# Optimization experiments

Measured on AMD Instinct MI355X. Metric: run time of the kernel, lower is better.

Reference implementation:

```python
import jax, jax.numpy as jnp
import numpy as np

NUM_NODES = 50000
NUM_EDGES = 800000
NUM_GRAPHS = 1024
D_IN = 64
D_PROT = 1280
HID = 256
OUT = 1


def setup_inputs() -> dict:
    key = jax.random.key(0)
    ks = jax.random.split(key, 16)
    s = 0.02
    x = jax.random.normal(ks[0], (NUM_NODES, D_IN), dtype=jnp.float32)
    edge_index = jax.random.randint(ks[1], (2, NUM_EDGES), 0, NUM_NODES, dtype=jnp.int32)
    batch = jnp.sort(jax.random.randint(ks[2], (NUM_NODES,), 0, NUM_GRAPHS, dtype=jnp.int32))
    protein_embedding = jax.random.normal(ks[3], (NUM_GRAPHS, D_PROT), dtype=jnp.float32)
    # SAGEConv params: lin_l (aggregated neighbors, with bias), lin_r (self, no bias)
    Wl = jax.random.normal(ks[4], (D_IN, HID), dtype=jnp.float32) * s
    bl = jnp.zeros((HID,), dtype=jnp.float32)
    Wr = jax.random.normal(ks[5], (D_IN, HID), dtype=jnp.float32) * s
    Wp = jax.random.normal(ks[6], (D_PROT, HID), dtype=jnp.float32) * s
    bp = jnp.zeros((HID,), dtype=jnp.float32)
    Wi = jax.random.normal(ks[7], (2 * HID, HID), dtype=jnp.float32) * s
    bi = jnp.zeros((HID,), dtype=jnp.float32)
    Wo = jax.random.normal(ks[8], (HID, OUT), dtype=jnp.float32) * s
    bo = jnp.zeros((OUT,), dtype=jnp.float32)
    return {"x": x, "protein_embedding": protein_embedding, "Wl": Wl, "bl": bl,
            "Wr": Wr, "Wp": Wp, "bp": bp, "Wi": Wi, "bi": bi, "Wo": Wo, "bo": bo,
            "edge_index": edge_index, "batch": batch}


def _segment_mean(vals, seg_ids, num_segments):
    sums = jax.ops.segment_sum(vals, seg_ids, num_segments=num_segments)
    cnt = jax.ops.segment_sum(jnp.ones((vals.shape[0],), vals.dtype), seg_ids,
                              num_segments=num_segments)
    return sums / jnp.maximum(cnt, 1.0)[:, None]


def reference(x, protein_embedding, Wl, bl, Wr, Wp, bp, Wi, bi, Wo, bo, edge_index, batch):
    src, dst = edge_index[0], edge_index[1]
    # SAGEConv: mean-aggregate neighbor messages at target nodes, then fuse linears
    aggr = _segment_mean(x[src], dst, NUM_NODES)           # [N, D_IN]
    drug_x = jax.nn.relu(aggr @ Wl + bl + x @ Wr)          # [N, HID]
    # global_mean_pool over graphs in the batch
    pooled = _segment_mean(drug_x, batch, NUM_GRAPHS)      # [G, HID]
    protein_x = protein_embedding @ Wp + bp                # [G, HID]
    combined = jnp.concatenate((pooled, protein_x), axis=1)  # [G, 2*HID]
    interaction = jax.nn.relu(combined @ Wi + bi)          # [G, HID]
    return interaction @ Wo + bo                           # [G, OUT]
```

## Files before the change

### kernel.cpp

```cpp
#include <hip/hip_runtime.h>
#include <hip/hip_bf16.h>

#define N_NODES 50000
#define N_EDGES 800000
#define N_GRAPHS 1024
#define D_IN 64
#define D_PROT 1280
#define HID 256
#define N_PAD 50048

#define NB 782
#define BCAP 2048
#define BEPB 4096
#define BBLK 196

typedef __attribute__((ext_vector_type(8))) short short8;
typedef __attribute__((ext_vector_type(4))) float f32x4;
typedef __hip_bfloat16 bf16;

__device__ inline unsigned bf16rne(float f) {
  unsigned u = __float_as_uint(f);
  return (u + 0x7fffu + ((u >> 16) & 1u)) >> 16;
}
__device__ inline void acc_bf2(float4& a, uint2 v) {
  a.x += __uint_as_float(v.x << 16);
  a.y += __uint_as_float(v.x & 0xffff0000u);
  a.z += __uint_as_float(v.y << 16);
  a.w += __uint_as_float(v.y & 0xffff0000u);
}

#define PREP_XC 3125
#define PREP_PE (PREP_XC + 1280)
#define PREP_PL (PREP_PE + 8)
#define PREP_PR (PREP_PL + 8)
#define PREP_WP (PREP_PR + 160)
#define PREP_WI (PREP_WP + 64)

__device__ inline void pack_frag(const float* __restrict__ src, bf16* __restrict__ dst,
                                 int KC, int tid) {
  int lane = tid & 63;
  int chunk = tid >> 6;
  int c = chunk / KC, kc = chunk - c * KC;
  int kbase = kc * 32 + ((lane >> 4) * 8);
  int n = c * 16 + (lane & 15);
#pragma unroll
  for (int j = 0; j < 8; ++j)
    dst[(size_t)tid * 8 + j] = __float2bfloat16(src[(size_t)(kbase + j) * HID + n]);
}

__global__ __launch_bounds__(256) void k_front(
    const float* __restrict__ x, const float* __restrict__ pe,
    const float* __restrict__ Wl, const float* __restrict__ Wr,
    const float* __restrict__ Wp, const float* __restrict__ Wi,
    const int* __restrict__ ei,
    uint2* __restrict__ x2, uint2* __restrict__ pe2,
    bf16* __restrict__ Wl_pk, bf16* __restrict__ Wr_pk,
    bf16* __restrict__ Wp_pk, bf16* __restrict__ Wi_pk,
    int* __restrict__ bcnt, unsigned* __restrict__ bped) {
  __shared__ int hist[NB];
  __shared__ int base[NB];
  const int b = blockIdx.x;
  const int t = threadIdx.x;
  if (b < BBLK) {
    const int e0 = b * BEPB;
    for (int i = t; i < NB; i += 256) hist[i] = 0;
    __syncthreads();
    for (int i = t; i < BEPB; i += 1024) {
      int d[4]; bool v[4];
#pragma unroll
      for (int u = 0; u < 4; ++u) {
        int idx = i + u * 256;
        v[u] = (e0 + idx < N_EDGES);
        d[u] = v[u] ? ei[N_EDGES + e0 + idx] : 0;
      }
#pragma unroll
      for (int u = 0; u < 4; ++u)
        if (v[u]) atomicAdd(&hist[d[u] >> 6], 1);
    }
    __syncthreads();
    for (int i = t; i < NB; i += 256) {
      int c = hist[i];
      base[i] = (c > 0) ? atomicAdd(&bcnt[i], c) : 0;
      hist[i] = 0;
    }
    __syncthreads();
    for (int i = t; i < BEPB; i += 1024) {
      int s[4], d[4]; bool v[4];
#pragma unroll
      for (int u = 0; u < 4; ++u) {
        int idx = i + u * 256;
        v[u] = (e0 + idx < N_EDGES);
        s[u] = v[u] ? ei[e0 + idx] : 0;
        d[u] = v[u] ? ei[N_EDGES + e0 + idx] : 0;
      }
#pragma unroll
      for (int u = 0; u < 4; ++u) {
        if (v[u]) {
          int bk = d[u] >> 6;
          int pos = base[bk] + atomicAdd(&hist[bk], 1);
          if (pos < BCAP)
            bped[(size_t)bk * BCAP + pos] =
                (unsigned)s[u] | ((unsigned)(d[u] & 63) << 16);
        }
      }
    }
    return;
  }
  const int pb = b - BBLK;
  if (pb < PREP_XC) {
    int tid = pb * 256 + t;
    float4 v = ((const float4*)x)[tid];
    x2[tid] = make_uint2(bf16rne(v.x) | (bf16rne(v.y) << 16),
                         bf16rne(v.z) | (bf16rne(v.w) << 16));
  } else if (pb < PREP_PE) {
    int tid = (pb - PREP_XC) * 256 + t;
    float4 v = ((const float4*)pe)[tid];
    pe2[tid] = make_uint2(bf16rne(v.x) | (bf16rne(v.y) << 16),
                          bf16rne(v.z) | (bf16rne(v.w) << 16));
  } else if (pb < PREP_PL) {
    pack_frag(Wl, Wl_pk, 2, (pb - PREP_PE) * 256 + t);
  } else if (pb < PREP_PR) {
    pack_frag(Wr, Wr_pk, 2, (pb - PREP_PL) * 256 + t);
  } else if (pb < PREP_WP) {
    pack_frag(Wp, Wp_pk, 40, (pb - PREP_PR) * 256 + t);
  } else {
    pack_frag(Wi, Wi_pk, 16, (pb - PREP_WP) * 256 + t);
  }
}

__global__ __launch_bounds__(256) void k_mid(
    const uint2* __restrict__ x2, const unsigned* __restrict__ bped,
    const int* __restrict__ bcnt, uint2* __restrict__ a2,
    const bf16* __restrict__ pebf, const bf16* __restrict__ Wp_pk,
    float* __restrict__ prot4) {
  __shared__ unsigned s_raw[BCAP];
  __shared__ unsigned short s_e[BCAP];
  __shared__ int s_off[65];
  __shared__ int s_cur[64];
  const int t = threadIdx.x;
  if (blockIdx.x < NB) {
    const int b = blockIdx.x;
    const int nE = min(bcnt[b], BCAP);
    if (t < 64) s_cur[t] = 0;
    __syncthreads();
    for (int i = t; i < nE; i += 256) {
      unsigned pk = bped[(size_t)b * BCAP + i];
      s_raw[i] = pk;
      atomicAdd(&s_cur[(pk >> 16) & 63], 1);
    }
    __syncthreads();
    if (t < 64) {
      int sc = s_cur[t];
#pragma unroll
      for (int off = 1; off < 64; off <<= 1) {
        int u = __shfl_up(sc, off);
        if (t >= off) sc += u;
      }
      s_off[t + 1] = sc;
      if (t == 0) s_off[0] = 0;
      s_cur[t] = 0;
    }
    __syncthreads();
    for (int i = t; i < nE; i += 256) {
      unsigned pk = s_raw[i];
      int ld = (pk >> 16) & 63;
      int pos = s_off[ld] + atomicAdd(&s_cur[ld], 1);
      s_e[pos] = (unsigned short)(pk & 0xffffu);
    }
    __syncthreads();

    const int w = t >> 6, lane = t & 63;
    const int el = lane >> 4;
    const int fb = lane & 15;
    for (int n = w; n < 64; n += 4) {
      const int beg = s_off[n], end = s_off[n + 1];
      float4 s0 = {0,0,0,0}, s1 = {0,0,0,0}, s2 = {0,0,0,0}, s3 = {0,0,0,0};
      int e = beg;
      for (; e + 16 <= end; e += 16) {
        int i0 = s_e[e + el],     i1 = s_e[e + 4 + el];
        int i2 = s_e[e + 8 + el], i3 = s_e[e + 12 + el];
        uint2 v0 = x2[(size_t)i0 * 16 + fb];
        uint2 v1 = x2[(size_t)i1 * 16 + fb];
        uint2 v2 = x2[(size_t)i2 * 16 + fb];
        uint2 v3 = x2[(size_t)i3 * 16 + fb];
        acc_bf2(s0, v0); acc_bf2(s1, v1); acc_bf2(s2, v2); acc_bf2(s3, v3);
      }
      for (; e + 4 <= end; e += 4)
        acc_bf2(s0, x2[(size_t)s_e[e + el] * 16 + fb]);
      if (e + el < end)
        acc_bf2(s1, x2[(size_t)s_e[e + el] * 16 + fb]);
      float4 tt;
      tt.x = (s0.x + s1.x) + (s2.x + s3.x);
      tt.y = (s0.y + s1.y) + (s2.y + s3.y);
      tt.z = (s0.z + s1.z) + (s2.z + s3.z);
      tt.w = (s0.w + s1.w) + (s2.w + s3.w);
      tt.x += __shfl_xor(tt.x, 32); tt.x += __shfl_xor(tt.x, 16);
      tt.y += __shfl_xor(tt.y, 32); tt.y += __shfl_xor(tt.y, 16);
      tt.z += __shfl_xor(tt.z, 32); tt.z += __shfl_xor(tt.z, 16);
      tt.w += __shfl_xor(tt.w, 32); tt.w += __shfl_xor(tt.w, 16);
      const int node = b * 64 + n;
      if (el == 0 && node < N_NODES) {
        float inv = 1.0f / (float)max(end - beg, 1);
        uint2 o;
        o.x = bf16rne(tt.x * inv) | (bf16rne(tt.y * inv) << 16);
        o.y = bf16rne(tt.z * inv) | (bf16rne(tt.w * inv) << 16);
        a2[(size_t)node * 16 + fb] = o;
      }
    }
    return;
  }
  const int kb = blockIdx.x - NB;
  const int w = t >> 6, lane = t & 63;
  const int ml = lane & 15, q = lane >> 4;
  const int mt = kb >> 2, ks = kb & 3;
  const int g0 = mt * 16, kc0 = ks * 10;
  f32x4 acc[4];
#pragma unroll
  for (int c = 0; c < 4; ++c) acc[c] = (f32x4){0.f, 0.f, 0.f, 0.f};
  for (int kc = kc0; kc < kc0 + 10; ++kc) {
    short8 a = *(const short8*)(pebf + (size_t)(g0 + ml) * D_PROT + kc * 32 + q * 8);
#pragma unroll
    for (int cl = 0; cl < 4; ++cl) {
      short8 bb = *(const short8*)(Wp_pk + ((size_t)((w * 4 + cl) * 40 + kc) * 64 + lane) * 8);
      acc[cl] = __builtin_amdgcn_mfma_f32_16x16x32_bf16(a, bb, acc[cl], 0, 0, 0);
    }
  }
#pragma unroll
  for (int cl = 0; cl < 4; ++cl) {
    const int col = w * 64 + cl * 16 + ml;
#pragma unroll
    for (int i = 0; i < 4; ++i)
      prot4[((size_t)ks * N_GRAPHS + g0 + q * 4 + i) * HID + col] = acc[cl][i];
  }
}

__global__ __launch_bounds__(256) void k_mlp(
    const bf16* __restrict__ aggrbf, const bf16* __restrict__ xbf,
    const bf16* __restrict__ Wl_pk, const bf16* __restrict__ Wr_pk,
    const float* __restrict__ bl, unsigned short* __restrict__ drug) {
  const int t = threadIdx.x, w = t >> 6, lane = t & 63;
  const int ml = lane & 15, q = lane >> 4;
  const int n0 = blockIdx.x * 64;

  f32x4 acc[4][4];
#pragma unroll
  for (int a = 0; a < 4; ++a)
#pragma unroll
    for (int c = 0; c < 4; ++c) acc[a][c] = (f32x4){0.f, 0.f, 0.f, 0.f};

#pragma unroll
  for (int mat = 0; mat < 2; ++mat) {
    const bf16* A = mat ? xbf : aggrbf;
    const bf16* B = mat ? Wr_pk : Wl_pk;
#pragma unroll
    for (int kc = 0; kc < 2; ++kc) {
      short8 af[4], bfr[4];
#pragma unroll
      for (int rt = 0; rt < 4; ++rt)
        af[rt] = *(const short8*)(A + (size_t)(n0 + rt * 16 + ml) * D_IN + kc * 32 + q * 8);
#pragma unroll
      for (int cl = 0; cl < 4; ++cl)
        bfr[cl] = *(const short8*)(B + ((size_t)((w * 4 + cl) * 2 + kc) * 64 + lane) * 8);
#pragma unroll
      for (int rt = 0; rt < 4; ++rt)
#pragma unroll
        for (int cl = 0; cl < 4; ++cl)
          acc[rt][cl] = __builtin_amdgcn_mfma_f32_16x16x32_bf16(af[rt], bfr[cl], acc[rt][cl], 0, 0, 0);
    }
  }

#pragma unroll
  for (int cl = 0; cl < 4; ++cl) {
    const int col = w * 64 + cl * 16 + ml;
    const float bias = bl[col];
#pragma unroll
    for (int rt = 0; rt < 4; ++rt) {
#pragma unroll
      for (int i = 0; i < 4; ++i) {
        const int row = n0 + rt * 16 + q * 4 + i;
        drug[(size_t)row * HID + col] =
            (unsigned short)bf16rne(fmaxf(acc[rt][cl][i] + bias, 0.f));
      }
    }
  }
}

__device__ inline int lb_dev(const int* __restrict__ a, int v) {
  int lo = 0, hi = N_NODES;
  while (lo < hi) { int m = (lo + hi) >> 1; if (a[m] < v) lo = m + 1; else hi = m; }
  return lo;
}

__global__ __launch_bounds__(256) void k_pool(
    const unsigned short* __restrict__ drug, const int* __restrict__ batch,
    const float* __restrict__ prot4, const float* __restrict__ bp,
    unsigned short* __restrict__ comb) {
  const int t = threadIdx.x;
  if (blockIdx.x < N_GRAPHS) {
    const int g = blockIdx.x;
    const int lo = lb_dev(batch, g);
    const int hi = lb_dev(batch, g + 1);
    float s0 = 0.f, s1 = 0.f, s2 = 0.f, s3 = 0.f;
    float s4 = 0.f, s5 = 0.f, s6 = 0.f, s7 = 0.f;
    int r = lo;
    for (; r + 8 <= hi; r += 8) {
      s0 += __uint_as_float((unsigned)drug[(size_t)(r + 0) * HID + t] << 16);
      s1 += __uint_as_float((unsigned)drug[(size_t)(r + 1) * HID + t] << 16);
      s2 += __uint_as_float((unsigned)drug[(size_t)(r + 2) * HID + t] << 16);
      s3 += __uint_as_float((unsigned)drug[(size_t)(r + 3) * HID + t] << 16);
      s4 += __uint_as_float((unsigned)drug[(size_t)(r + 4) * HID + t] << 16);
      s5 += __uint_as_float((unsigned)drug[(size_t)(r + 5) * HID + t] << 16);
      s6 += __uint_as_float((unsigned)drug[(size_t)(r + 6) * HID + t] << 16);
      s7 += __uint_as_float((unsigned)drug[(size_t)(r + 7) * HID + t] << 16);
    }
    for (; r < hi; ++r)
      s0 += __uint_as_float((unsigned)drug[(size_t)r * HID + t] << 16);
    float inv = 1.0f / (float)max(hi - lo, 1);
    float m = (((s0 + s1) + (s2 + s3)) + ((s4 + s5) + (s6 + s7))) * inv;
    comb[(size_t)g * 512 + t] = (unsigned short)bf16rne(m);
    return;
  }
  const int pb = blockIdx.x - N_GRAPHS;
#pragma unroll
  for (int g = 0; g < 4; ++g) {
    const int gg = pb * 4 + g;
    size_t idx = (size_t)gg * HID + t;
    float pr = prot4[idx] + prot4[(size_t)N_GRAPHS * HID + idx]
             + prot4[2 * (size_t)N_GRAPHS * HID + idx]
             + prot4[3 * (size_t)N_GRAPHS * HID + idx];
    comb[(size_t)gg * 512 + HID + t] = (unsigned short)bf16rne(pr + bp[t]);
  }
}

__global__ __launch_bounds__(256) void k_tail(
    const bf16* __restrict__ comb, const bf16* __restrict__ Wi_pk,
    const float* __restrict__ bi, const float* __restrict__ Wo,
    const float* __restrict__ bo, float* __restrict__ out) {
  __shared__ float sRed[16 * 4];
  const int t = threadIdx.x, w = t >> 6, lane = t & 63;
  const int ml = lane & 15, q = lane >> 4;
  const int g0 = blockIdx.x * 16;
  f32x4 acc[4];
#pragma unroll
  for (int c = 0; c < 4; ++c) acc[c] = (f32x4){0.f, 0.f, 0.f, 0.f};
  for (int kc = 0; kc < 16; ++kc) {
    short8 a = *(const short8*)(comb + (size_t)(g0 + ml) * 512 + kc * 32 + q * 8);
#pragma unroll
    for (int cl = 0; cl < 4; ++cl) {
      short8 bb = *(const short8*)(Wi_pk + ((size_t)((w * 4 + cl) * 16 + kc) * 64 + lane) * 8);
      acc[cl] = __builtin_amdgcn_mfma_f32_16x16x32_bf16(a, bb, acc[cl], 0, 0, 0);
    }
  }
  float bic[4], woc[4];
#pragma unroll
  for (int cl = 0; cl < 4; ++cl) {
    const int col = w * 64 + cl * 16 + ml;
    bic[cl] = bi[col];
    woc[cl] = Wo[col];
  }
#pragma unroll
  for (int i = 0; i < 4; ++i) {
    float s = 0.f;
#pragma unroll
    for (int cl = 0; cl < 4; ++cl)
      s += fmaxf(acc[cl][i] + bic[cl], 0.f) * woc[cl];
    s += __shfl_xor(s, 1); s += __shfl_xor(s, 2);
    s += __shfl_xor(s, 4); s += __shfl_xor(s, 8);
    if (ml == 0) sRed[(q * 4 + i) * 4 + w] = s;
  }
  __syncthreads();
  if (t < 16)
    out[g0 + t] = sRed[t * 4 + 0] + sRed[t * 4 + 1] + sRed[t * 4 + 2]
                + sRed[t * 4 + 3] + bo[0];
}

extern "C" void kernel_launch(void* const* d_in, const int* in_sizes, int n_in,
                              void* d_out, int out_size, void* d_ws, size_t ws_size,
                              hipStream_t stream) {
  const float* x     = (const float*)d_in[0];
  const float* pe    = (const float*)d_in[1];
  const float* Wl    = (const float*)d_in[2];
  const float* bl    = (const float*)d_in[3];
  const float* Wr    = (const float*)d_in[4];
  const float* Wp    = (const float*)d_in[5];
  const float* bp    = (const float*)d_in[6];
  const float* Wi    = (const float*)d_in[7];
  const float* bi    = (const float*)d_in[8];
  const float* Wo    = (const float*)d_in[9];
  const float* bo    = (const float*)d_in[10];
  const int*   ei    = (const int*)d_in[11];
  const int*   batch = (const int*)d_in[12];
  float* out = (float*)d_out;

  char* p = (char*)d_ws;
  auto alloc = [&](size_t bytes) {
    char* r = p;
    p += (bytes + 255) & ~(size_t)255;
    return r;
  };
  int*      bcnt  = (int*)alloc(NB * 4);
  size_t zbytes = (size_t)(p - (char*)d_ws);
  unsigned* bped  = (unsigned*)alloc((size_t)NB * BCAP * 4);
  bf16*  xbf    = (bf16*)alloc((size_t)N_PAD * D_IN * 2);
  bf16*  aggrbf = (bf16*)alloc((size_t)N_PAD * D_IN * 2);
  bf16*  pebf   = (bf16*)alloc((size_t)N_GRAPHS * D_PROT * 2);
  bf16*  Wl_pk  = (bf16*)alloc((size_t)D_IN * HID * 2);
  bf16*  Wr_pk  = (bf16*)alloc((size_t)D_IN * HID * 2);
  bf16*  Wp_pk  = (bf16*)alloc((size_t)D_PROT * HID * 2);
  bf16*  Wi_pk  = (bf16*)alloc((size_t)2 * HID * HID * 2);
  float* prot4  = (float*)alloc((size_t)4 * N_GRAPHS * HID * 4);
  unsigned short* drug = (unsigned short*)alloc((size_t)N_PAD * HID * 2);
  unsigned short* comb = (unsigned short*)alloc((size_t)N_GRAPHS * 2 * HID * 2);

  (void)hipMemsetAsync(d_ws, 0, zbytes, stream);

  k_front<<<BBLK + PREP_WI, 256, 0, stream>>>(
      x, pe, Wl, Wr, Wp, Wi, ei,
      (uint2*)xbf, (uint2*)pebf, Wl_pk, Wr_pk, Wp_pk, Wi_pk, bcnt, bped);
  k_mid<<<NB + 256, 256, 0, stream>>>(
      (const uint2*)xbf, bped, bcnt, (uint2*)aggrbf, pebf, Wp_pk, prot4);
  k_mlp<<<N_PAD / 64, 256, 0, stream>>>(aggrbf, xbf, Wl_pk, Wr_pk, bl, drug);
  k_pool<<<N_GRAPHS + 256, 256, 0, stream>>>(drug, batch, prot4, bp, comb);
  k_tail<<<N_GRAPHS / 16, 256, 0, stream>>>((const bf16*)comb, Wi_pk, bi, Wo, bo, out);
}
```

Before: 173.2 us.

## Fuse SAGE linear and mean pooling into aggregation kernel via atomics

The aggregation kernel now keeps the per-node mean aggregate in shared memory and immediately runs the Wl/Wr MFMA GEMM, applying bias and ReLU. It then reduces rows per graph and atomically adds them into a float pool-sum buffer. The protein-sum and mean normalization are folded into the tail kernel, which builds the combined row tile in LDS. This removes the aggr, drug and comb intermediate buffers and two kernel launches, in exchange for more LDS and register pressure in k_mid and contention from atomic adds into poolsum.

New measurement: 167.4 us. 3.3% less time.

```diff
diff --git a/kernel.cpp b/kernel.cpp
--- a/kernel.cpp
+++ b/kernel.cpp
@@ -128,18 +128,23 @@
   }
 }
 
-__global__ __launch_bounds__(256) void k_mid(
+__global__ __launch_bounds__(256, 4) void k_mid(
     const uint2* __restrict__ x2, const unsigned* __restrict__ bped,
-    const int* __restrict__ bcnt, uint2* __restrict__ a2,
+    const int* __restrict__ bcnt, const int* __restrict__ batch,
+    const bf16* __restrict__ Wl_pk, const bf16* __restrict__ Wr_pk,
+    const float* __restrict__ bl, float* __restrict__ poolsum,
     const bf16* __restrict__ pebf, const bf16* __restrict__ Wp_pk,
     float* __restrict__ prot4) {
-  __shared__ unsigned s_raw[BCAP];
+  __shared__ unsigned s_raw[2304];
   __shared__ unsigned short s_e[BCAP];
   __shared__ int s_off[65];
   __shared__ int s_cur[64];
+  __shared__ int s_batch[64];
   const int t = threadIdx.x;
   if (blockIdx.x < NB) {
+    uint2* aggT = (uint2*)s_raw;
     const int b = blockIdx.x;
+    const int n0 = b * 64;
     const int nE = min(bcnt[b], BCAP);
     if (t < 64) s_cur[t] = 0;
     __syncthreads();
@@ -166,6 +171,10 @@
       int ld = (pk >> 16) & 63;
       int pos = s_off[ld] + atomicAdd(&s_cur[ld], 1);
       s_e[pos] = (unsigned short)(pk & 0xffffu);
+    }
+    if (t < 64) {
+      int node = n0 + t;
+      s_batch[t] = (node < N_NODES) ? batch[node] : 0x7fffffff;
     }
     __syncthreads();
 
@@ -198,13 +207,63 @@
       tt.y += __shfl_xor(tt.y, 32); tt.y += __shfl_xor(tt.y, 16);
       tt.z += __shfl_xor(tt.z, 32); tt.z += __shfl_xor(tt.z, 16);
       tt.w += __shfl_xor(tt.w, 32); tt.w += __shfl_xor(tt.w, 16);
-      const int node = b * 64 + n;
-      if (el == 0 && node < N_NODES) {
+      if (el == 0) {
         float inv = 1.0f / (float)max(end - beg, 1);
         uint2 o;
         o.x = bf16rne(tt.x * inv) | (bf16rne(tt.y * inv) << 16);
         o.y = bf16rne(tt.z * inv) | (bf16rne(tt.w * inv) << 16);
-        a2[(size_t)node * 16 + fb] = o;
+        aggT[n * 18 + fb] = o;
+      }
+    }
+    __syncthreads();
+
+    const int ml = lane & 15, q = lane >> 4;
+    const int lv = min(63, N_NODES - 1 - n0);
+    float bic[4];
+#pragma unroll
+    for (int cl = 0; cl < 4; ++cl) bic[cl] = bl[w * 64 + cl * 16 + ml];
+#pragma unroll
+    for (int rt = 0; rt < 4; ++rt) {
+      f32x4 acc[4];
+#pragma unroll
+      for (int cl = 0; cl < 4; ++cl) acc[cl] = (f32x4){0.f, 0.f, 0.f, 0.f};
+      const int arow = rt * 16 + ml;
+#pragma unroll
+      for (int kc = 0; kc < 2; ++kc) {
+        short8 a0 = *(const short8*)(&aggT[arow * 18 + kc * 8 + q * 2]);
+#pragma unroll
+        for (int cl = 0; cl < 4; ++cl) {
+          short8 bb = *(const short8*)(Wl_pk + ((size_t)((w * 4 + cl) * 2 + kc) * 64 + lane) * 8);
+          acc[cl] = __builtin_amdgcn_mfma_f32_16x16x32_bf16(a0, bb, acc[cl], 0, 0, 0);
+        }
+        short8 a1 = *(const short8*)((const bf16*)x2 + (size_t)(n0 + arow) * D_IN + kc * 32 + q * 8);
+#pragma unroll
+        for (int cl = 0; cl < 4; ++cl) {
+          short8 bb = *(const short8*)(Wr_pk + ((size_t)((w * 4 + cl) * 2 + kc) * 64 + lane) * 8);
+          acc[cl] = __builtin_amdgcn_mfma_f32_16x16x32_bf16(a1, bb, acc[cl], 0, 0, 0);
+        }
+      }
+      float vv[4][4];
+      int bt[4];
+#pragma unroll
+      for (int i = 0; i < 4; ++i) bt[i] = s_batch[rt * 16 + q * 4 + i];
+#pragma unroll
+      for (int cl = 0; cl < 4; ++cl)
+#pragma unroll
+        for (int i = 0; i < 4; ++i)
+          vv[cl][i] = fmaxf(acc[cl][i] + bic[cl], 0.f);
+      const int glo = s_batch[min(rt * 16, lv)];
+      const int ghi = s_batch[min(rt * 16 + 15, lv)];
+      for (int g = glo; g <= ghi; ++g) {
+#pragma unroll
+        for (int cl = 0; cl < 4; ++cl) {
+          float s = 0.f;
+#pragma unroll
+          for (int i = 0; i < 4; ++i) s += (bt[i] == g) ? vv[cl][i] : 0.f;
+          s += __shfl_xor(s, 16); s += __shfl_xor(s, 32);
+          if (q == 0)
+            atomicAdd(&poolsum[(size_t)g * HID + (w * 64 + cl * 16 + ml)], s);
+        }
       }
     }
     return;
@@ -234,117 +293,49 @@
   }
 }
 
-__global__ __launch_bounds__(256) void k_mlp(
-    const bf16* __restrict__ aggrbf, const bf16* __restrict__ xbf,
-    const bf16* __restrict__ Wl_pk, const bf16* __restrict__ Wr_pk,
-    const float* __restrict__ bl, unsigned short* __restrict__ drug) {
-  const int t = threadIdx.x, w = t >> 6, lane = t & 63;
-  const int ml = lane & 15, q = lane >> 4;
-  const int n0 = blockIdx.x * 64;
-
-  f32x4 acc[4][4];
-#pragma unroll
-  for (int a = 0; a < 4; ++a)
-#pragma unroll
-    for (int c = 0; c < 4; ++c) acc[a][c] = (f32x4){0.f, 0.f, 0.f, 0.f};
-
-#pragma unroll
-  for (int mat = 0; mat < 2; ++mat) {
-    const bf16* A = mat ? xbf : aggrbf;
-    const bf16* B = mat ? Wr_pk : Wl_pk;
-#pragma unroll
-    for (int kc = 0; kc < 2; ++kc) {
-      short8 af[4], bfr[4];
-#pragma unroll
-      for (int rt = 0; rt < 4; ++rt)
-        af[rt] = *(const short8*)(A + (size_t)(n0 + rt * 16 + ml) * D_IN + kc * 32 + q * 8);
-#pragma unroll
-      for (int cl = 0; cl < 4; ++cl)
-        bfr[cl] = *(const short8*)(B + ((size_t)((w * 4 + cl) * 2 + kc) * 64 + lane) * 8);
-#pragma unroll
-      for (int rt = 0; rt < 4; ++rt)
-#pragma unroll
-        for (int cl = 0; cl < 4; ++cl)
-          acc[rt][cl] = __builtin_amdgcn_mfma_f32_16x16x32_bf16(af[rt], bfr[cl], acc[rt][cl], 0, 0, 0);
-    }
-  }
-
-#pragma unroll
-  for (int cl = 0; cl < 4; ++cl) {
-    const int col = w * 64 + cl * 16 + ml;
-    const float bias = bl[col];
-#pragma unroll
-    for (int rt = 0; rt < 4; ++rt) {
-#pragma unroll
-      for (int i = 0; i < 4; ++i) {
-        const int row = n0 + rt * 16 + q * 4 + i;
-        drug[(size_t)row * HID + col] =
-            (unsigned short)bf16rne(fmaxf(acc[rt][cl][i] + bias, 0.f));
-      }
-    }
-  }
-}
-
 __device__ inline int lb_dev(const int* __restrict__ a, int v) {
   int lo = 0, hi = N_NODES;
   while (lo < hi) { int m = (lo + hi) >> 1; if (a[m] < v) lo = m + 1; else hi = m; }
   return lo;
 }
 
-__global__ __launch_bounds__(256) void k_pool(
-    const unsigned short* __restrict__ drug, const int* __restrict__ batch,
+__global__ __launch_bounds__(256) void k_tail(
+    const float* __restrict__ poolsum, const int* __restrict__ batch,
     const float* __restrict__ prot4, const float* __restrict__ bp,
-    unsigned short* __restrict__ comb) {
-  const int t = threadIdx.x;
-  if (blockIdx.x < N_GRAPHS) {
-    const int g = blockIdx.x;
-    const int lo = lb_dev(batch, g);
-    const int hi = lb_dev(batch, g + 1);
-    float s0 = 0.f, s1 = 0.f, s2 = 0.f, s3 = 0.f;
-    float s4 = 0.f, s5 = 0.f, s6 = 0.f, s7 = 0.f;
-    int r = lo;
-    for (; r + 8 <= hi; r += 8) {
-      s0 += __uint_as_float((unsigned)drug[(size_t)(r + 0) * HID + t] << 16);
-      s1 += __uint_as_float((unsigned)drug[(size_t)(r + 1) * HID + t] << 16);
-      s2 += __uint_as_float((unsigned)drug[(size_t)(r + 2) * HID + t] << 16);
-      s3 += __uint_as_float((unsigned)drug[(size_t)(r + 3) * HID + t] << 16);
-      s4 += __uint_as_float((unsigned)drug[(size_t)(r + 4) * HID + t] << 16);
-      s5 += __uint_as_float((unsigned)drug[(size_t)(r + 5) * HID + t] << 16);
-      s6 += __uint_as_float((unsigned)drug[(size_t)(r + 6) * HID + t] << 16);
-      s7 += __uint_as_float((unsigned)drug[(size_t)(r + 7) * HID + t] << 16);
-    }
-    for (; r < hi; ++r)
-      s0 += __uint_as_float((unsigned)drug[(size_t)r * HID + t] << 16);
-    float inv = 1.0f / (float)max(hi - lo, 1);
-    float m = (((s0 + s1) + (s2 + s3)) + ((s4 + s5) + (s6 + s7))) * inv;
-    comb[(size_t)g * 512 + t] = (unsigned short)bf16rne(m);
-    return;
-  }
-  const int pb = blockIdx.x - N_GRAPHS;
-#pragma unroll
-  for (int g = 0; g < 4; ++g) {
-    const int gg = pb * 4 + g;
-    size_t idx = (size_t)gg * HID + t;
-    float pr = prot4[idx] + prot4[(size_t)N_GRAPHS * HID + idx]
-             + prot4[2 * (size_t)N_GRAPHS * HID + idx]
-             + prot4[3 * (size_t)N_GRAPHS * HID + idx];
-    comb[(size_t)gg * 512 + HID + t] = (unsigned short)bf16rne(pr + bp[t]);
-  }
-}
-
-__global__ __launch_bounds__(256) void k_tail(
-    const bf16* __restrict__ comb, const bf16* __restrict__ Wi_pk,
-    const float* __restrict__ bi, const float* __restrict__ Wo,
-    const float* __restrict__ bo, float* __restrict__ out) {
+    const bf16* __restrict__ Wi_pk, const float* __restrict__ bi,
+    const float* __restrict__ Wo, const float* __restrict__ bo,
+    float* __restrict__ out) {
+  __shared__ bf16 aT[16][520];
+  __shared__ float s_inv[16];
   __shared__ float sRed[16 * 4];
   const int t = threadIdx.x, w = t >> 6, lane = t & 63;
   const int ml = lane & 15, q = lane >> 4;
   const int g0 = blockIdx.x * 16;
+  if (t < 16) {
+    int lo = lb_dev(batch, g0 + t), hi = lb_dev(batch, g0 + t + 1);
+    s_inv[t] = 1.0f / (float)max(hi - lo, 1);
+  }
+  __syncthreads();
+  for (int idx = t; idx < 16 * 512; idx += 256) {
+    const int row = idx >> 9, col = idx & 511;
+    float v;
+    if (col < HID) {
+      v = poolsum[(size_t)(g0 + row) * HID + col] * s_inv[row];
+    } else {
+      const int c = col - HID;
+      const size_t base = (size_t)(g0 + row) * HID + c;
+      v = prot4[base] + prot4[(size_t)N_GRAPHS * HID + base]
+        + prot4[2 * (size_t)N_GRAPHS * HID + base]
+        + prot4[3 * (size_t)N_GRAPHS * HID + base] + bp[c];
+    }
+    aT[row][col] = __float2bfloat16(v);
+  }
+  __syncthreads();
   f32x4 acc[4];
 #pragma unroll
   for (int c = 0; c < 4; ++c) acc[c] = (f32x4){0.f, 0.f, 0.f, 0.f};
   for (int kc = 0; kc < 16; ++kc) {
-    short8 a = *(const short8*)(comb + (size_t)(g0 + ml) * 512 + kc * 32 + q * 8);
+    short8 a = *(const short8*)(&aT[ml][kc * 32 + q * 8]);
 #pragma unroll
     for (int cl = 0; cl < 4; ++cl) {
       short8 bb = *(const short8*)(Wi_pk + ((size_t)((w * 4 + cl) * 16 + kc) * 64 + lane) * 8);
@@ -398,19 +389,17 @@
     p += (bytes + 255) & ~(size_t)255;
     return r;
   };
-  int*      bcnt  = (int*)alloc(NB * 4);
+  int*   bcnt    = (int*)alloc(NB * 4);
+  float* poolsum = (float*)alloc((size_t)N_GRAPHS * HID * 4);
   size_t zbytes = (size_t)(p - (char*)d_ws);
   unsigned* bped  = (unsigned*)alloc((size_t)NB * BCAP * 4);
   bf16*  xbf    = (bf16*)alloc((size_t)N_PAD * D_IN * 2);
-  bf16*  aggrbf = (bf16*)alloc((size_t)N_PAD * D_IN * 2);
   bf16*  pebf   = (bf16*)alloc((size_t)N_GRAPHS * D_PROT * 2);
   bf16*  Wl_pk  = (bf16*)alloc((size_t)D_IN * HID * 2);
   bf16*  Wr_pk  = (bf16*)alloc((size_t)D_IN * HID * 2);
   bf16*  Wp_pk  = (bf16*)alloc((size_t)D_PROT * HID * 2);
   bf16*  Wi_pk  = (bf16*)alloc((size_t)2 * HID * HID * 2);
   float* prot4  = (float*)alloc((size_t)4 * N_GRAPHS * HID * 4);
-  unsigned short* drug = (unsigned short*)alloc((size_t)N_PAD * HID * 2);
-  unsigned short* comb = (unsigned short*)alloc((size_t)N_GRAPHS * 2 * HID * 2);
 
   (void)hipMemsetAsync(d_ws, 0, zbytes, stream);
 
@@ -418,8 +407,8 @@
       x, pe, Wl, Wr, Wp, Wi, ei,
       (uint2*)xbf, (uint2*)pebf, Wl_pk, Wr_pk, Wp_pk, Wi_pk, bcnt, bped);
   k_mid<<<NB + 256, 256, 0, stream>>>(
-      (const uint2*)xbf, bped, bcnt, (uint2*)aggrbf, pebf, Wp_pk, prot4);
-  k_mlp<<<N_PAD / 64, 256, 0, stream>>>(aggrbf, xbf, Wl_pk, Wr_pk, bl, drug);
-  k_pool<<<N_GRAPHS + 256, 256, 0, stream>>>(drug, batch, prot4, bp, comb);
-  k_tail<<<N_GRAPHS / 16, 256, 0, stream>>>((const bf16*)comb, Wi_pk, bi, Wo, bo, out);
-}
+      (const uint2*)xbf, bped, bcnt, batch, Wl_pk, Wr_pk, bl, poolsum,
+      pebf, Wp_pk, prot4);
+  k_tail<<<N_GRAPHS / 16, 256, 0, stream>>>(
+      poolsum, batch, prot4, bp, Wi_pk, bi, Wo, bo, out);
+}
```
